# Optimization experiments

Hardware: AMD Instinct MI355X
Metric: run time of the kernel (lower is better)

## Reference

```python
import jax, jax.numpy as jnp
import numpy as np

N_NODES = 100000
EMB_DIM = 128
N_EDGES = 500000
N_REL = 16
SYM_IDX = [0, 2, 4, 6]
EPS = 1e-8


def setup_inputs() -> dict:
    key = jax.random.key(0)
    k1, k2, k3, k4 = jax.random.split(key, 4)
    node_embeddings = jax.random.normal(k1, (N_NODES, EMB_DIM), dtype=jnp.float32)
    edge_index = jax.random.randint(k2, (2, N_EDGES), 0, N_NODES)
    relation_type = jax.random.randint(k3, (N_EDGES,), 0, N_REL)
    # relation embedding table [num_relations, embedding_dim//2]:
    # symmetric rows set to -1.0, asymmetric rows uniform(-pi, pi) (phases)
    rel = jax.random.uniform(k4, (N_REL, EMB_DIM // 2), dtype=jnp.float32,
                             minval=-np.pi, maxval=np.pi)
    sym = np.zeros(N_REL, dtype=bool)
    sym[SYM_IDX] = True
    relation_emb = jnp.where(jnp.asarray(sym)[:, None], jnp.float32(-1.0), rel)
    return {
        "node_embeddings": node_embeddings,
        "relation_emb": relation_emb,
        "edge_index": edge_index,
        "relation_type": relation_type,
    }


def reference(node_embeddings, relation_emb, edge_index, relation_type):
    is_symmetric = jnp.zeros(N_REL, dtype=bool).at[jnp.array(SYM_IDX)].set(True)
    # F.normalize(p=2, dim=1) with torch default eps=1e-12
    norm = jnp.linalg.norm(node_embeddings, axis=1, keepdims=True)
    x = node_embeddings / jnp.maximum(norm, 1e-12)

    h = x[edge_index[0]]  # [E, D]
    t = x[edge_index[1]]  # [E, D]

    # DotProduct branch: score = -(1 - mean(h * t))
    dot_score = -(1.0 - jnp.mean(h * t, axis=1))

    # RotatE branch: complex rotation of head by relation phase, L2 distance to tail
    half = EMB_DIM // 2
    phase = relation_emb[relation_type]          # [E, D/2]
    c, s = jnp.cos(phase), jnp.sin(phase)
    h_re, h_im = h[:, :half], h[:, half:]
    t_re, t_im = t[:, :half], t[:, half:]
    d_re = h_re * c - h_im * s - t_re
    d_im = h_re * s + h_im * c - t_im
    dist = jnp.sqrt(jnp.sum(d_re * d_re + d_im * d_im, axis=1) + EPS)
    rot_score = -dist

    sym_mask = is_symmetric[relation_type]       # [E]
    return jnp.where(sym_mask, dot_score, rot_score)
```

## Files before the change

### kernel.cpp

```cpp
#include <hip/hip_runtime.h>
#include <hip/hip_fp16.h>
#include <hip/hip_fp8.h>
#include <math.h>

#define N_NODES 100000
#define EMB_DIM 128
#define HALF    64
#define N_EDGES 500000
#define N_REL   16

__global__ void build_trig_interleaved(const float* __restrict__ rel_emb,
                                       float* __restrict__ trig) {
    int idx = blockIdx.x * blockDim.x + threadIdx.x;
    if (idx < N_REL * HALF) {
        int r = idx >> 6, d = idx & 63;
        float p = rel_emb[idx];
        trig[r * 128 + 2 * d]     = cosf(p);
        trig[r * 128 + 2 * d + 1] = sinf(p);
    }
}

__device__ __forceinline__ unsigned short enc2(float a, float b) {
    __hip_fp8x2_e4m3 f(float2{a, b});
    return (unsigned short)f.__x;
}
__device__ __forceinline__ float2 dec2(unsigned short v) {
    __hip_fp8x2_e4m3 f;
    f.__x = (__hip_fp8x2_storage_t)v;
    return (float2)f;
}

__global__ __launch_bounds__(256) void normalize_fp8(
    const float* __restrict__ emb, unsigned int* __restrict__ tab) {
    int row  = blockIdx.x * 8 + (threadIdx.x >> 5);
    int l    = threadIdx.x & 31;
    if (row >= N_NODES) return;
    const float* rp = emb + (size_t)row * EMB_DIM;
    float2 re = *(const float2*)(rp + 2 * l);
    float2 im = *(const float2*)(rp + HALF + 2 * l);
    float p = re.x * re.x + re.y * re.y + im.x * im.x + im.y * im.y;
    for (int m = 16; m >= 1; m >>= 1) p += __shfl_xor(p, m);
    float rn = 1.0f / fmaxf(sqrtf(p), 1e-12f);
    unsigned int w = (unsigned int)enc2(re.x * rn, im.x * rn)
                   | ((unsigned int)enc2(re.y * rn, im.y * rn) << 16);
    __builtin_nontemporal_store(w, tab + (size_t)row * 32 + l);
}

__global__ __launch_bounds__(256) void rotate_edge_fp8(
    const unsigned int* __restrict__ tab,
    const float* __restrict__ trig,
    const int* __restrict__ eidx,
    const int* __restrict__ rtype,
    float* __restrict__ out)
{
    int e   = (blockIdx.x * blockDim.x + threadIdx.x) >> 3;
    int sub = threadIdx.x & 7;
    if (e >= N_EDGES) return;

    int hidx = eidx[e];
    int tidx = eidx[N_EDGES + e];
    int r    = rtype[e];

    uint4 hv = ((const uint4*)(tab + (size_t)hidx * 32))[sub];
    uint4 tv = ((const uint4*)(tab + (size_t)tidx * 32))[sub];
    const float4* tg = ((const float4*)(trig + r * 128)) + 4 * sub;

    float dot = 0.f, cx = 0.f;
#define DOPAIR(HW, TW, TG) {                                           \
        float2 h0 = dec2((unsigned short)((HW) & 0xffff));             \
        float2 h1 = dec2((unsigned short)((HW) >> 16));                \
        float2 t0 = dec2((unsigned short)((TW) & 0xffff));             \
        float2 t1 = dec2((unsigned short)((TW) >> 16));                \
        dot += h0.x * t0.x + h0.y * t0.y + h1.x * t1.x + h1.y * t1.y;  \
        cx  += (h0.x * (TG).x - h0.y * (TG).y) * t0.x                  \
             + (h0.x * (TG).y + h0.y * (TG).x) * t0.y;                 \
        cx  += (h1.x * (TG).z - h1.y * (TG).w) * t1.x                  \
             + (h1.x * (TG).w + h1.y * (TG).z) * t1.y;                 \
    }
    DOPAIR(hv.x, tv.x, tg[0])
    DOPAIR(hv.y, tv.y, tg[1])
    DOPAIR(hv.z, tv.z, tg[2])
    DOPAIR(hv.w, tv.w, tg[3])
#undef DOPAIR

    for (int m = 4; m >= 1; m >>= 1) {
        dot += __shfl_xor(dot, m);
        cx  += __shfl_xor(cx, m);
    }

    if (sub == 0) {
        float dot_score = dot * (1.0f / (float)EMB_DIM) - 1.0f;
        float d2 = fmaxf(2.0f - 2.0f * cx, 0.0f) + 1e-8f;
        float rot_score = -sqrtf(d2);
        bool sym = (r == 0) | (r == 2) | (r == 4) | (r == 6);
        out[e] = sym ? dot_score : rot_score;
    }
}

__global__ __launch_bounds__(256) void normalize_fp16_rowmajor(
    const float* __restrict__ emb, unsigned int* __restrict__ tab) {
    int row  = blockIdx.x * 4 + (threadIdx.x >> 6);
    int lane = threadIdx.x & 63;
    if (row >= N_NODES) return;
    const float* rp = emb + (size_t)row * EMB_DIM;
    float a = rp[lane];
    float b = rp[lane + HALF];
    float p = a * a + b * b;
    for (int m = 32; m >= 1; m >>= 1) p += __shfl_xor(p, m);
    float rn = 1.0f / fmaxf(sqrtf(p), 1e-12f);
    __half2 hv = __floats2half2_rn(a * rn, b * rn);
    tab[(size_t)row * 64 + lane] = *reinterpret_cast<unsigned int*>(&hv);
}

__device__ __forceinline__ float2 u2f2(unsigned int u) {
    __half2 h = *reinterpret_cast<const __half2*>(&u);
    return __half22float2(h);
}

__global__ __launch_bounds__(256) void rotate_edge_fp16(
    const unsigned int* __restrict__ tab,
    const float* __restrict__ trig,
    const int* __restrict__ eidx,
    const int* __restrict__ rtype,
    float* __restrict__ out)
{
    int e   = (blockIdx.x * blockDim.x + threadIdx.x) >> 4;
    int sub = threadIdx.x & 15;
    if (e >= N_EDGES) return;
    int hidx = eidx[e];
    int tidx = eidx[N_EDGES + e];
    int r    = rtype[e];
    uint4 hv = ((const uint4*)(tab + (size_t)hidx * 64))[sub];
    uint4 tv = ((const uint4*)(tab + (size_t)tidx * 64))[sub];
    const float4* cp = (const float4*)(trig + r * 128);
    float4 c0 = cp[2 * sub];
    float4 c1 = cp[2 * sub + 1];
    float dot = 0.f, cx = 0.f;
#define PAIR(HU, TU, CC, SS) {                               \
        float2 h2 = u2f2(HU);                                \
        float2 t2 = u2f2(TU);                                \
        dot += h2.x * t2.x + h2.y * t2.y;                    \
        float rr = h2.x * (CC) - h2.y * (SS);                \
        float ri = h2.x * (SS) + h2.y * (CC);                \
        cx += rr * t2.x + ri * t2.y;                         \
    }
    PAIR(hv.x, tv.x, c0.x, c0.y)
    PAIR(hv.y, tv.y, c0.z, c0.w)
    PAIR(hv.z, tv.z, c1.x, c1.y)
    PAIR(hv.w, tv.w, c1.z, c1.w)
#undef PAIR
    for (int m = 8; m >= 1; m >>= 1) {
        dot += __shfl_xor(dot, m);
        cx  += __shfl_xor(cx, m);
    }
    if (sub == 0) {
        float dot_score = dot * (1.0f / (float)EMB_DIM) - 1.0f;
        float d2 = fmaxf(2.0f - 2.0f * cx, 0.0f) + 1e-8f;
        float rot_score = -sqrtf(d2);
        bool sym = (r == 0) | (r == 2) | (r == 4) | (r == 6);
        out[e] = sym ? dot_score : rot_score;
    }
}

extern "C" void kernel_launch(void* const* d_in, const int* in_sizes, int n_in,
                              void* d_out, int out_size, void* d_ws, size_t ws_size,
                              hipStream_t stream) {
    const float* emb   = (const float*)d_in[0];
    const float* rel   = (const float*)d_in[1];
    const int*   eidx  = (const int*)d_in[2];
    const int*   rtype = (const int*)d_in[3];
    float*       out   = (float*)d_out;

    const size_t trig_bytes = (size_t)N_REL * 128 * sizeof(float);
    const size_t tab8_bytes = (size_t)N_NODES * 32 * sizeof(unsigned int);
    const size_t tab16_bytes= (size_t)N_NODES * 64 * sizeof(unsigned int);

    if (ws_size >= trig_bytes + tab8_bytes) {
        float*        trig = (float*)d_ws;
        unsigned int* tab  = (unsigned int*)((char*)d_ws + trig_bytes);

        build_trig_interleaved<<<(N_REL * HALF + 255) / 256, 256, 0, stream>>>(rel, trig);
        normalize_fp8<<<(N_NODES + 7) / 8, 256, 0, stream>>>(emb, tab);
        int blocks = (N_EDGES * 8 + 255) / 256;
        rotate_edge_fp8<<<blocks, 256, 0, stream>>>(tab, trig, eidx, rtype, out);
    } else if (ws_size >= trig_bytes + tab16_bytes) {
        float*        trig = (float*)d_ws;
        unsigned int* tab  = (unsigned int*)((char*)d_ws + trig_bytes);
        build_trig_interleaved<<<(N_REL * HALF + 255) / 256, 256, 0, stream>>>(rel, trig);
        normalize_fp16_rowmajor<<<(N_NODES + 3) / 4, 256, 0, stream>>>(emb, tab);
        int blocks = (N_EDGES * 16 + 255) / 256;
        rotate_edge_fp16<<<blocks, 256, 0, stream>>>(tab, trig, eidx, rtype, out);
    }
}
```

Baseline: 46.26 us.

## Fuse trig table build into normalize kernel and stage trig in LDS

The cos/sin table construction moves into an extra block of the normalization kernel, removing one kernel launch. The edge kernel copies the 8 KB trig table into padded shared memory per block and reads the rotation coefficients from LDS instead of global memory. Edge index, relation and output accesses switch to nontemporal loads and stores. The trade-off is a per-block LDS fill plus a __syncthreads in the edge kernel, which has many small blocks.

```diff
diff --git a/kernel.cpp b/kernel.cpp
--- a/kernel.cpp
+++ b/kernel.cpp
@@ -8,17 +8,7 @@
 #define HALF    64
 #define N_EDGES 500000
 #define N_REL   16
-
-__global__ void build_trig_interleaved(const float* __restrict__ rel_emb,
-                                       float* __restrict__ trig) {
-    int idx = blockIdx.x * blockDim.x + threadIdx.x;
-    if (idx < N_REL * HALF) {
-        int r = idx >> 6, d = idx & 63;
-        float p = rel_emb[idx];
-        trig[r * 128 + 2 * d]     = cosf(p);
-        trig[r * 128 + 2 * d + 1] = sinf(p);
-    }
-}
+#define TRIG_STRIDE 132
 
 __device__ __forceinline__ unsigned short enc2(float a, float b) {
     __hip_fp8x2_e4m3 f(float2{a, b});
@@ -30,8 +20,18 @@
     return (float2)f;
 }
 
-__global__ __launch_bounds__(256) void normalize_fp8(
-    const float* __restrict__ emb, unsigned int* __restrict__ tab) {
+__global__ __launch_bounds__(256) void normalize_fp8_and_trig(
+    const float* __restrict__ emb, const float* __restrict__ rel_emb,
+    unsigned int* __restrict__ tab, float* __restrict__ trig) {
+    if (blockIdx.x == gridDim.x - 1) {
+        for (int i = threadIdx.x; i < N_REL * HALF; i += 256) {
+            int r = i >> 6, d = i & 63;
+            float p = rel_emb[i];
+            trig[r * 128 + 2 * d]     = cosf(p);
+            trig[r * 128 + 2 * d + 1] = sinf(p);
+        }
+        return;
+    }
     int row  = blockIdx.x * 8 + (threadIdx.x >> 5);
     int l    = threadIdx.x & 31;
     if (row >= N_NODES) return;
@@ -53,17 +53,30 @@
     const int* __restrict__ rtype,
     float* __restrict__ out)
 {
+    __shared__ float strig[N_REL * TRIG_STRIDE];
+
+    {
+        int t = threadIdx.x;
+        int r = t >> 4, off = (t & 15) * 8;
+        const float4* g = (const float4*)(trig + r * 128 + off);
+        float4 a = g[0], b = g[1];
+        float* d = strig + r * TRIG_STRIDE + off;
+        *(float4*)(d)     = a;
+        *(float4*)(d + 4) = b;
+    }
+    __syncthreads();
+
     int e   = (blockIdx.x * blockDim.x + threadIdx.x) >> 3;
     int sub = threadIdx.x & 7;
     if (e >= N_EDGES) return;
 
-    int hidx = eidx[e];
-    int tidx = eidx[N_EDGES + e];
-    int r    = rtype[e];
+    int hidx = __builtin_nontemporal_load(eidx + e);
+    int tidx = __builtin_nontemporal_load(eidx + N_EDGES + e);
+    int r    = __builtin_nontemporal_load(rtype + e);
 
     uint4 hv = ((const uint4*)(tab + (size_t)hidx * 32))[sub];
     uint4 tv = ((const uint4*)(tab + (size_t)tidx * 32))[sub];
-    const float4* tg = ((const float4*)(trig + r * 128)) + 4 * sub;
+    const float4* tg = (const float4*)(strig + r * TRIG_STRIDE + 16 * sub);
 
     float dot = 0.f, cx = 0.f;
 #define DOPAIR(HW, TW, TG) {                                           \
@@ -93,7 +106,18 @@
         float d2 = fmaxf(2.0f - 2.0f * cx, 0.0f) + 1e-8f;
         float rot_score = -sqrtf(d2);
         bool sym = (r == 0) | (r == 2) | (r == 4) | (r == 6);
-        out[e] = sym ? dot_score : rot_score;
+        __builtin_nontemporal_store(sym ? dot_score : rot_score, out + e);
+    }
+}
+
+__global__ void build_trig_interleaved(const float* __restrict__ rel_emb,
+                                       float* __restrict__ trig) {
+    int idx = blockIdx.x * blockDim.x + threadIdx.x;
+    if (idx < N_REL * HALF) {
+        int r = idx >> 6, d = idx & 63;
+        float p = rel_emb[idx];
+        trig[r * 128 + 2 * d]     = cosf(p);
+        trig[r * 128 + 2 * d + 1] = sinf(p);
     }
 }
 
@@ -171,16 +195,16 @@
     const int*   rtype = (const int*)d_in[3];
     float*       out   = (float*)d_out;
 
-    const size_t trig_bytes = (size_t)N_REL * 128 * sizeof(float);
-    const size_t tab8_bytes = (size_t)N_NODES * 32 * sizeof(unsigned int);
-    const size_t tab16_bytes= (size_t)N_NODES * 64 * sizeof(unsigned int);
+    const size_t trig_bytes  = (size_t)N_REL * 128 * sizeof(float);
+    const size_t tab8_bytes  = (size_t)N_NODES * 32 * sizeof(unsigned int);
+    const size_t tab16_bytes = (size_t)N_NODES * 64 * sizeof(unsigned int);
 
     if (ws_size >= trig_bytes + tab8_bytes) {
         float*        trig = (float*)d_ws;
         unsigned int* tab  = (unsigned int*)((char*)d_ws + trig_bytes);
 
-        build_trig_interleaved<<<(N_REL * HALF + 255) / 256, 256, 0, stream>>>(rel, trig);
-        normalize_fp8<<<(N_NODES + 7) / 8, 256, 0, stream>>>(emb, tab);
+        int nblocks = (N_NODES + 7) / 8 + 1;
+        normalize_fp8_and_trig<<<nblocks, 256, 0, stream>>>(emb, rel, tab, trig);
         int blocks = (N_EDGES * 8 + 255) / 256;
         rotate_edge_fp8<<<blocks, 256, 0, stream>>>(tab, trig, eidx, rtype, out);
     } else if (ws_size >= trig_bytes + tab16_bytes) {
```

After: 41.67 us. 9.9% less time.
